# Kernel tuning notes

Hardware: AMD Instinct MI355X
Metric: run time of the kernel (lower is better)

## Reference

```python
import jax, jax.numpy as jnp
import numpy as np

N_NODES = 10000
N_EDGES = 160000
MUL = 16            # multiplicity: emb_dim=64, max_l=1 -> irreps 16x0e + 16x1o
EMB = 64
NUM_BASIS = 10
MAX_RADIUS = 4.5
HIDDEN = 64
N_PATHS = 4         # (0e,0e->0e), (0e,1o->1o), (1o,0e->1o), (1o,1o->0e)
W_NUMEL = N_PATHS * MUL * MUL  # 1024


def setup_inputs() -> dict:
    key = jax.random.key(0)
    ks = jax.random.split(key, 6)
    x = jax.random.normal(ks[0], (N_NODES, EMB), jnp.float32)
    src = jax.random.randint(ks[1], (N_EDGES,), 0, N_NODES)
    dst = jax.random.randint(ks[2], (N_EDGES,), 0, N_NODES)
    edge_vec = jax.random.normal(ks[3], (N_EDGES, 3), jnp.float32)
    mlp_w1 = jax.random.normal(ks[4], (NUM_BASIS, HIDDEN), jnp.float32)
    mlp_w2 = jax.random.normal(ks[5], (HIDDEN, W_NUMEL), jnp.float32)
    return {"x": x, "edge_vec": edge_vec, "mlp_w1": mlp_w1,
            "mlp_w2": mlp_w2, "src": src, "dst": dst}


def _sus(t):
    # e3nn smooth bump helper: exp(-1/t) for t>0 else 0
    return jnp.where(t > 0, jnp.exp(-1.0 / jnp.where(t > 0, t, 1.0)), 0.0)


def _radial_embedding(r):
    # soft_one_hot_linspace(basis='smooth_finite', cutoff=True), then *sqrt(num_basis)
    values = jnp.linspace(0.0, MAX_RADIUS, NUM_BASIS + 2)[1:-1]
    step = MAX_RADIUS / (NUM_BASIS + 1)
    diff = (r[:, None] - values) / step                     # [E, NUM_BASIS]
    basis = 1.14136 * jnp.exp(2.0) * _sus(diff + 1.0) * _sus(1.0 - diff)
    return basis * (NUM_BASIS ** 0.5)


def _forward(x, edge_vec, mlp_w1, mlp_w2, src, dst):
    E = edge_vec.shape[0]
    N = x.shape[0]
    r = jnp.linalg.norm(edge_vec, axis=1)                   # [E]
    # spherical harmonics, lmax=1, normalize=True, 'component' norm: Y0=1, Y1=sqrt(3)*n
    y1 = jnp.sqrt(3.0) * edge_vec / r[:, None]              # [E, 3]

    # radial MLP (e3nn FullyConnectedNet: W~N(0,1), x@W/sqrt(fan_in), relu scaled by sqrt(2))
    emb = _radial_embedding(r)                              # [E, 10]
    h = jnp.sqrt(2.0) * jax.nn.relu(emb @ (mlp_w1 / NUM_BASIS ** 0.5))
    w = h @ (mlp_w2 / HIDDEN ** 0.5)                        # [E, 1024]
    w = w.reshape(E, N_PATHS, MUL, MUL)                     # paths in e3nn order A,B,C,D

    xs = x[src]                                             # gather [E, 64]
    x0 = xs[:, :MUL]                                        # [E, 16] 0e scalars
    x1 = xs[:, MUL:].reshape(E, MUL, 3)                     # [E, 16, 3] 1o vectors

    # Fully connected TP normalization ('component', path_norm 'element'):
    # out0 fan = 2*MUL -> alpha 1/(2*MUL); out1 alpha 3/(2*MUL) with w3j 1/sqrt(3)
    c = 1.0 / jnp.sqrt(2.0 * MUL)
    inv_sqrt3 = 1.0 / jnp.sqrt(3.0)
    wA, wB, wC, wD = w[:, 0], w[:, 1], w[:, 2], w[:, 3]
    # 0e outputs: 0e*0e->0e and 1o*1o->0e (dot product, w3j = I/sqrt(3))
    out0 = c * (jnp.einsum('euw,eu->ew', wA, x0)
                + inv_sqrt3 * jnp.einsum('euw,eum,em->ew', wD, x1, y1))
    # 1o outputs: 0e*1o->1o and 1o*0e->1o (w3j = I/sqrt(3), Y0 = 1)
    out1 = c * (jnp.einsum('euw,eu,em->ewm', wB, x0, y1)
                + jnp.einsum('euw,eum->ewm', wC, x1))
    summand = jnp.concatenate([out0, out1.reshape(E, MUL * 3)], axis=1)  # [E, 64]

    out = jax.ops.segment_sum(summand, dst, num_segments=N)             # [N, 64]
    return out * (N / E)


def reference(x, edge_vec, mlp_w1, mlp_w2, src, dst):
    return _forward(x, edge_vec, mlp_w1, mlp_w2, src, dst)
```

## Files before the change

### kernel.cpp

```cpp
#include <hip/hip_runtime.h>
#include <hip/hip_bf16.h>


typedef __attribute__((ext_vector_type(8))) short bf16x8;
typedef __attribute__((ext_vector_type(8))) unsigned short u16x8;
typedef __attribute__((ext_vector_type(4))) float f32x4;

#define NN 10000
#define NE 160000

__device__ __forceinline__ float sus_f(float t) { return t > 0.0f ? __expf(-1.0f / t) : 0.0f; }
__device__ __forceinline__ unsigned int f2bf(float f) {
    unsigned int u = __float_as_uint(f);
    u += 0x7FFFu + ((u >> 16) & 1u);
    return u >> 16;
}
__device__ __forceinline__ float bf2f(unsigned short v) { return __uint_as_float(((unsigned int)v) << 16); }
__device__ __forceinline__ float bflo(unsigned int v) { return __uint_as_float(v << 16); }
__device__ __forceinline__ float bfhi(unsigned int v) { return __uint_as_float(v & 0xFFFF0000u); }
__device__ __forceinline__ float bfe(u16x8 v, int i) { return __uint_as_float(((unsigned int)v[i]) << 16); }

#define GL16(g, l) __builtin_amdgcn_global_load_lds( \
    (const __attribute__((address_space(1))) void*)(g), \
    (__attribute__((address_space(3))) void*)(l), 16, 0, 0)

__device__ __forceinline__ void stageN(const void* g, void* l, int bytes, int tid, int nthr) {
    const char* gc = (const char*)g;
    char* lc = (char*)l;
    const int units = bytes >> 4;
    for (int u = tid; u < units; u += nthr) GL16(gc + ((long)u << 4), lc + (u << 4));
}

__global__ void hist_k(const int* __restrict__ dst, int* __restrict__ hist,
                       const float* __restrict__ w2, char* __restrict__ w2bf) {
    if (blockIdx.x < 625) {
        const int e = blockIdx.x * 256 + threadIdx.x;
        if (e < NE) atomicAdd(&hist[dst[e]], 1);
    } else {
        const int idx = (blockIdx.x - 625) * 256 + threadIdx.x;
        const int j = idx >> 10, R = idx & 1023;
        unsigned int pk[4];
        #pragma unroll
        for (int p = 0; p < 4; ++p) {
            const unsigned int lo = f2bf(w2[(size_t)(8 * j + 2 * p) * 1024 + R]);
            const unsigned int hi = f2bf(w2[(size_t)(8 * j + 2 * p + 1) * 1024 + R]);
            pk[p] = lo | (hi << 16);
        }
        uint4 v; v.x = pk[0]; v.y = pk[1]; v.z = pk[2]; v.w = pk[3];
        *(uint4*)(w2bf + R * 128 + ((j ^ (R & 7)) << 4)) = v;
    }
}

__global__ __launch_bounds__(1024) void scan_k(const int* __restrict__ hist,
                                               int* __restrict__ offsets) {
    __shared__ int hl[NN];
    __shared__ int wsum[16];
    const int tid = threadIdx.x;
    for (int i = tid; i < NN; i += 1024) hl[i] = hist[i];
    __syncthreads();
    const int base = tid * 10;
    int loc[10]; int s = 0;
    #pragma unroll
    for (int i = 0; i < 10; ++i) { loc[i] = s; const int b = base + i; s += (b < NN) ? hl[b] : 0; }
    int v = s;
    const int lane = tid & 63, wv = tid >> 6;
    #pragma unroll
    for (int d = 1; d < 64; d <<= 1) { int t2 = __shfl_up(v, d); if (lane >= d) v += t2; }
    if (lane == 63) wsum[wv] = v;
    __syncthreads();
    if (tid < 64) {
        int w = (tid < 16) ? wsum[tid] : 0;
        #pragma unroll
        for (int d = 1; d < 16; d <<= 1) { int t2 = __shfl_up(w, d); if (tid >= d) w += t2; }
        if (tid < 16) wsum[tid] = w;
    }
    __syncthreads();
    const int wexc = (wv == 0) ? 0 : wsum[wv - 1];
    const int texc = wexc + v - s;
    #pragma unroll
    for (int i = 0; i < 10; ++i) { const int b = base + i; if (b < NN) offsets[b] = texc + loc[i]; }
    if (tid == 1023) offsets[NN] = texc + s;
}

__global__ void scatter_k(const int* __restrict__ dst, const int* __restrict__ src,
                          const int* __restrict__ offsets,
                          int* __restrict__ cursor, int* __restrict__ perm,
                          int* __restrict__ dsts, int* __restrict__ srcg) {
    const int e = blockIdx.x * 256 + threadIdx.x;
    if (e < NE) {
        const int d = dst[e];
        const int pos = offsets[d] + atomicAdd(&cursor[d], 1);
        perm[pos] = e;
        dsts[pos] = d;
        if (srcg) srcg[pos] = src[e];
    }
}

__global__ __launch_bounds__(512, 2) void se3_edge(
    const char* __restrict__ w2bf, const float* __restrict__ x,
    const float* __restrict__ edge_vec, const float* __restrict__ w1,
    const int* __restrict__ perm, const int* __restrict__ srcg,
    const int* __restrict__ dsts, float* __restrict__ out)
{
    __shared__ __align__(16) char w2lds[65536];
    __shared__ __align__(16) char x0l[4096];
    __shared__ __align__(16) char x1Tl[16384];
    __shared__ float y1l[128][4];
    __shared__ float embl[128][10];
    __shared__ __align__(16) float w1l[640];
    __shared__ __align__(16) int meta[1920];
    __shared__ __align__(16) char summb[12672];
    __shared__ int segst[2][66];
    __shared__ int nseg[2];

    const int tid = threadIdx.x, lane = tid & 63, wv = tid >> 6;
    const int lm = lane & 15, q = lane >> 4, erow = wv << 4;
    const int tb = blockIdx.x;
    const int pair = blockIdx.y;
    const int s0 = (q ^ (lm & 7)) << 4, s1 = s0 ^ 64;
    const int sel = tid >> 2, sa = tid & 3;
    const float S = 0.17677669529663687f * 0.125f * 0.0625f;
    const float C0 = 1.14136f * __expf(2.0f) * 3.1622776601683795f;
    const long e00 = (long)tb * 640;

    {
        const int pa = pair ? 1 : 0, pb = pair ? 2 : 3;
        stageN(w2bf + pa * 32768, w2lds, 32768, tid, 512);
        stageN(w2bf + pb * 32768, w2lds + 32768, 32768, tid, 512);
        stageN((const char*)(perm + e00), meta,        2560, tid, 512);
        stageN((const char*)(srcg + e00), meta + 640,  2560, tid, 512);
        stageN((const char*)(dsts + e00), meta + 1280, 2560, tid, 512);
        stageN((const char*)w1, w1l, 2560, tid, 512);
    }
    __syncthreads();

    const char* w2p0 = w2lds;
    const char* w2p1 = w2lds + 32768;
    const int arow = erow + lm;

    for (int tt = 0; tt < 5; ++tt) {
        const int eb = tt << 7;
        {
            const int eid = meta[eb + sel];
            const int s   = meta[640 + eb + sel];
            const float vx = edge_vec[eid * 3 + 0];
            const float vy = edge_vec[eid * 3 + 1];
            const float vz = edge_vec[eid * 3 + 2];
            const float r = sqrtf(vx * vx + vy * vy + vz * vz);
            if (sa == 0) {
                const float sc = 1.7320508075688772f / r;
                *(float4*)&y1l[sel][0] = make_float4(vx * sc, vy * sc, vz * sc, 0.f);
            }
            #pragma unroll
            for (int i = sa; i < 10; i += 4) {
                const float diff = r * (11.0f / 4.5f) - (float)(i + 1);
                embl[sel][i] = C0 * sus_f(diff + 1.0f) * sus_f(1.0f - diff);
            }
            const float4 v0 = *(const float4*)&x[(size_t)s * 64 + 4 * sa];
            uint2 p0;
            p0.x = f2bf(v0.x) | (f2bf(v0.y) << 16);
            p0.y = f2bf(v0.z) | (f2bf(v0.w) << 16);
            *(uint2*)(x0l + sel * 32 + sa * 8) = p0;
            const float* xp = &x[(size_t)s * 64 + 16 + 12 * sa];
            const float4 q0 = *(const float4*)xp;
            const float4 q1 = *(const float4*)(xp + 4);
            const float4 q2 = *(const float4*)(xp + 8);
            const float f[12] = { q0.x, q0.y, q0.z, q0.w, q1.x, q1.y,
                                  q1.z, q1.w, q2.x, q2.y, q2.z, q2.w };
            #pragma unroll
            for (int k = 0; k < 4; ++k) {
                uint2 v;
                v.x = f2bf(f[3 * k]) | (f2bf(f[3 * k + 1]) << 16);
                v.y = f2bf(f[3 * k + 2]);
                *(uint2*)(x1Tl + (((4 * sa + k) << 7) + sel) * 8) = v;
            }
        }
        __syncthreads();

        float ha[8], hb[8];
        #pragma unroll
        for (int jj = 0; jj < 8; ++jj) { ha[jj] = 0.f; hb[jj] = 0.f; }
        #pragma unroll
        for (int i = 0; i < 10; ++i) {
            const float ei = embl[arow][i];
            const float4 wa0 = *(const float4*)&w1l[i * 64 + 8 * q];
            const float4 wa1 = *(const float4*)&w1l[i * 64 + 8 * q + 4];
            const float4 wb0 = *(const float4*)&w1l[i * 64 + 32 + 8 * q];
            const float4 wb1 = *(const float4*)&w1l[i * 64 + 36 + 8 * q];
            ha[0] += ei * wa0.x; ha[1] += ei * wa0.y; ha[2] += ei * wa0.z; ha[3] += ei * wa0.w;
            ha[4] += ei * wa1.x; ha[5] += ei * wa1.y; ha[6] += ei * wa1.z; ha[7] += ei * wa1.w;
            hb[0] += ei * wb0.x; hb[1] += ei * wb0.y; hb[2] += ei * wb0.z; hb[3] += ei * wb0.w;
            hb[4] += ei * wb1.x; hb[5] += ei * wb1.y; hb[6] += ei * wb1.z; hb[7] += ei * wb1.w;
        }
        bf16x8 a0, a1;
        #pragma unroll
        for (int jj = 0; jj < 8; ++jj) {
            a0[jj] = (short)f2bf(fmaxf(ha[jj], 0.0f) * 0.4472135954999579f);
            a1[jj] = (short)f2bf(fmaxf(hb[jj], 0.0f) * 0.4472135954999579f);
        }

        u16x8 flo[4], fhi[4];
        float4 ye[4];
        #pragma unroll
        for (int r = 0; r < 4; ++r) {
            const int el = erow + 4 * q + r;
            flo[r] = *(const u16x8*)(x0l + el * 32);
            fhi[r] = *(const u16x8*)(x0l + el * 32 + 16);
            ye[r]  = *(const float4*)&y1l[el][0];
        }

        float ac0[4] = {0,0,0,0}, ac1[4] = {0,0,0,0}, ac2[4] = {0,0,0,0}, ac3[4] = {0,0,0,0};
        #pragma unroll
        for (int t = 0; t < 16; ++t) {
            const int rowb = (t * 16 + lm) << 7;
            const bf16x8 b00 = *(const bf16x8*)(w2p0 + rowb + s0);
            const bf16x8 b01 = *(const bf16x8*)(w2p0 + rowb + s1);
            const bf16x8 b10 = *(const bf16x8*)(w2p1 + rowb + s0);
            const bf16x8 b11 = *(const bf16x8*)(w2p1 + rowb + s1);
            f32x4 wP = {0.f,0.f,0.f,0.f}, wQ = {0.f,0.f,0.f,0.f};
            wP = __builtin_amdgcn_mfma_f32_16x16x32_bf16(a0, b00, wP, 0,0,0);
            wP = __builtin_amdgcn_mfma_f32_16x16x32_bf16(a1, b01, wP, 0,0,0);
            wQ = __builtin_amdgcn_mfma_f32_16x16x32_bf16(a0, b10, wQ, 0,0,0);
            wQ = __builtin_amdgcn_mfma_f32_16x16x32_bf16(a1, b11, wQ, 0,0,0);
            #pragma unroll
            for (int r = 0; r < 4; ++r) {
                const int el = erow + 4 * q + r;
                const uint2 xv = *(const uint2*)(x1Tl + (((t << 7) + el)) * 8);
                const float x0v = (t < 8) ? bfe(flo[r], t) : bfe(fhi[r], t - 8);
                ac0[r] += wP[r] * x0v;
                if (pair == 0) {
                    const float zv = bflo(xv.x) * ye[r].x + bfhi(xv.x) * ye[r].y
                                   + bflo(xv.y) * ye[r].z;
                    ac1[r] += wQ[r] * zv;
                } else {
                    ac1[r] += wQ[r] * bflo(xv.x);
                    ac2[r] += wQ[r] * bfhi(xv.x);
                    ac3[r] += wQ[r] * bflo(xv.y);
                }
            }
        }

        if (pair == 0) {
            float* summ32 = (float*)summb;
            #pragma unroll
            for (int r = 0; r < 4; ++r) {
                const int el = erow + 4 * q + r;
                summ32[lm * 132 + el] = S * (ac0[r] + 0.5773502691896258f * ac1[r]);
            }
        } else {
            unsigned short* summ16 = (unsigned short*)summb;
            #pragma unroll
            for (int r = 0; r < 4; ++r) {
                const int el = erow + 4 * q + r;
                const float b = S * ac0[r];
                summ16[(3 * lm + 0) * 132 + el] = (unsigned short)f2bf(b * ye[r].x + S * ac1[r]);
                summ16[(3 * lm + 1) * 132 + el] = (unsigned short)f2bf(b * ye[r].y + S * ac2[r]);
                summ16[(3 * lm + 2) * 132 + el] = (unsigned short)f2bf(b * ye[r].z + S * ac3[r]);
            }
        }
        const int* dstl = meta + 1280 + eb;
        if (wv < 2) {
            const int base = wv << 6;
            const int d = dstl[base + lane];
            const bool flag = (lane == 0) || (d != dstl[base + lane - 1]);
            const unsigned long long m = __ballot(flag);
            const int sid = (lane == 0) ? 0 : __popcll(m & ((1ull << lane) - 1ull));
            if (flag) segst[wv][sid] = base + lane;
            if (lane == 63) { const int ns = __popcll(m); nseg[wv] = ns; segst[wv][ns] = base + 64; }
        }
        __syncthreads();

        const int nsa = nseg[0], nsb = nseg[1];
        if (pair == 0) {
            const float* sm = (const float*)summb;
            const int total = (nsa + nsb) << 4;
            for (int i = tid; i < total; i += 512) {
                const int sg = i >> 4, c = i & 15;
                const int hh = (sg >= nsa) ? 1 : 0;
                const int sl = hh ? sg - nsa : sg;
                const int ebg = segst[hh][sl], ee = segst[hh][sl + 1];
                float s = 0.f;
                for (int e = ebg; e < ee; ++e) s += sm[c * 132 + e];
                atomicAdd(&out[(size_t)dstl[ebg] * 64 + c], s);
            }
        } else {
            const unsigned short* sm = (const unsigned short*)summb;
            const int total = (nsa + nsb) * 48;
            for (int i = tid; i < total; i += 512) {
                const int sg = i / 48, c = i - sg * 48;
                const int hh = (sg >= nsa) ? 1 : 0;
                const int sl = hh ? sg - nsa : sg;
                const int ebg = segst[hh][sl], ee = segst[hh][sl + 1];
                float s = 0.f;
                for (int e = ebg; e < ee; ++e) s += bf2f(sm[c * 132 + e]);
                atomicAdd(&out[(size_t)dstl[ebg] * 64 + 16 + c], s);
            }
        }
    }
}

#define FBT 64
template<int PATH>
__device__ __forceinline__ void fb_body(
    const float* __restrict__ x, const float* __restrict__ edge_vec,
    const float* __restrict__ w1, const float* __restrict__ w2,
    const int* __restrict__ src, const int* __restrict__ perm,
    const int* __restrict__ dsts, float* __restrict__ out,
    unsigned short (*w2t)[72], float* arena, float (*y1l)[4],
    int* dstl, int* srcl, int* segstart, int* nseg_s)
{
    constexpr int NC    = (PATH == 0 || PATH == 3) ? 16 : 48;
    constexpr int CBASE = (PATH == 0 || PATH == 3) ? 0 : 16;
    const int tid = threadIdx.x;
    float* embl = arena;
    unsigned short* hl = (unsigned short*)(arena + 640);
    float* feats = arena + 2944;
    float* summ  = arena;
    {
        const float* col = w2 + PATH * 256 + tid;
        #pragma unroll
        for (int k = 0; k < 64; k += 2) {
            const unsigned int lo = f2bf(col[(size_t)k * 1024]);
            const unsigned int hi = f2bf(col[(size_t)(k + 1) * 1024]);
            *(unsigned int*)&w2t[tid][k] = lo | (hi << 16);
        }
    }
    const int lane = tid & 63, wv = tid >> 6, lm = lane & 15, q = lane >> 4;
    const int erow = wv * 16;
    const float C0 = 1.14136f * __expf(2.0f) * 3.1622776601683795f;
    const float S  = 0.17677669529663687f * 0.125f * 0.0625f;
    for (int it = 0; it < 2; ++it) {
        const int e0 = (blockIdx.x * 2 + it) * FBT;
        __syncthreads();
        for (int idx = tid; idx < FBT * 10; idx += 256) {
            const int e = idx / 10, i = idx - e * 10;
            const int eid = perm[e0 + e];
            const float vx = edge_vec[eid * 3 + 0], vy = edge_vec[eid * 3 + 1], vz = edge_vec[eid * 3 + 2];
            const float r = sqrtf(vx * vx + vy * vy + vz * vz);
            const float diff = r * (11.0f / 4.5f) - (float)(i + 1);
            embl[e * 10 + i] = C0 * sus_f(diff + 1.0f) * sus_f(1.0f - diff);
            if (i == 0) {
                const float sc = 1.7320508075688772f / r;
                y1l[e][0] = vx * sc; y1l[e][1] = vy * sc; y1l[e][2] = vz * sc;
                dstl[e] = dsts[e0 + e];
                srcl[e] = src[eid];
            }
        }
        __syncthreads();
        for (int idx = tid; idx < FBT * 8; idx += 256) {
            const int e = idx >> 3, j0 = (idx & 7) * 8;
            float acc[8];
            #pragma unroll
            for (int j = 0; j < 8; ++j) acc[j] = 0.0f;
            #pragma unroll
            for (int i = 0; i < 10; ++i) {
                const float ei = embl[e * 10 + i];
                #pragma unroll
                for (int j = 0; j < 8; ++j) acc[j] += ei * w1[i * 64 + j0 + j];
            }
            unsigned int pk[4];
            #pragma unroll
            for (int p = 0; p < 4; ++p) {
                const unsigned int lo = f2bf(fmaxf(acc[2 * p],     0.0f) * 0.4472135954999579f);
                const unsigned int hi = f2bf(fmaxf(acc[2 * p + 1], 0.0f) * 0.4472135954999579f);
                pk[p] = lo | (hi << 16);
            }
            uint4 v; v.x = pk[0]; v.y = pk[1]; v.z = pk[2]; v.w = pk[3];
            *(uint4*)&hl[e * 72 + j0] = v;
        }
        if (PATH == 2) {
            for (int idx = tid; idx < FBT * 48; idx += 256) {
                const int e = idx / 48, c = idx - e * 48;
                feats[e * 48 + c] = x[(size_t)srcl[e] * 64 + 16 + c];
            }
        } else if (PATH == 3) {
            for (int idx = tid; idx < FBT * 16; idx += 256) {
                const int e = idx >> 4, u = idx & 15;
                const float* xs = x + (size_t)srcl[e] * 64 + 16 + u * 3;
                feats[e * 16 + u] = xs[0] * y1l[e][0] + xs[1] * y1l[e][1] + xs[2] * y1l[e][2];
            }
        } else {
            for (int idx = tid; idx < FBT * 16; idx += 256) {
                const int e = idx >> 4, u = idx & 15;
                feats[e * 16 + u] = x[(size_t)srcl[e] * 64 + u];
            }
        }
        __syncthreads();
        const bf16x8 a0 = *(const bf16x8*)&hl[(erow + lm) * 72 + 8 * q];
        const bf16x8 a1 = *(const bf16x8*)&hl[(erow + lm) * 72 + 32 + 8 * q];
        float accO[4] = {0.f,0.f,0.f,0.f}, accC0[4] = {0.f,0.f,0.f,0.f};
        float accC1[4] = {0.f,0.f,0.f,0.f}, accC2[4] = {0.f,0.f,0.f,0.f};
        #pragma unroll 4
        for (int t = 0; t < 16; ++t) {
            const bf16x8 b0 = *(const bf16x8*)&w2t[t * 16 + lm][8 * q];
            const bf16x8 b1 = *(const bf16x8*)&w2t[t * 16 + lm][32 + 8 * q];
            f32x4 wa = {0.f,0.f,0.f,0.f};
            wa = __builtin_amdgcn_mfma_f32_16x16x32_bf16(a0, b0, wa, 0, 0, 0);
            wa = __builtin_amdgcn_mfma_f32_16x16x32_bf16(a1, b1, wa, 0, 0, 0);
            #pragma unroll
            for (int r = 0; r < 4; ++r) {
                const int el = erow + 4 * q + r;
                if (PATH == 2) {
                    accC0[r] += wa[r] * feats[el * 48 + t * 3 + 0];
                    accC1[r] += wa[r] * feats[el * 48 + t * 3 + 1];
                    accC2[r] += wa[r] * feats[el * 48 + t * 3 + 2];
                } else {
                    accO[r] += wa[r] * feats[el * 16 + t];
                }
            }
        }
        __syncthreads();
        #pragma unroll
        for (int r = 0; r < 4; ++r) {
            const int el = erow + 4 * q + r;
            if (PATH == 0) summ[el * 16 + lm] = S * accO[r];
            else if (PATH == 3) summ[el * 16 + lm] = S * 0.5773502691896258f * accO[r];
            else if (PATH == 1) {
                const float tv = S * accO[r];
                summ[el * 48 + lm * 3 + 0] = tv * y1l[el][0];
                summ[el * 48 + lm * 3 + 1] = tv * y1l[el][1];
                summ[el * 48 + lm * 3 + 2] = tv * y1l[el][2];
            } else {
                summ[el * 48 + lm * 3 + 0] = S * accC0[r];
                summ[el * 48 + lm * 3 + 1] = S * accC1[r];
                summ[el * 48 + lm * 3 + 2] = S * accC2[r];
            }
        }
        if (tid < 64) {
            const int d = dstl[tid];
            const bool flag = (tid == 0) || (d != dstl[tid - 1]);
            const unsigned long long m = __ballot(flag);
            const int sid = (tid == 0) ? 0 : __popcll(m & ((1ull << tid) - 1ull));
            if (flag) segstart[sid] = tid;
            if (tid == 63) { const int ns = __popcll(m); *nseg_s = ns; segstart[ns] = 64; }
        }
        __syncthreads();
        const int ns = *nseg_s;
        for (int i = tid; i < ns * NC; i += 256) {
            const int s = i / NC, c = i - s * NC;
            const int eb = segstart[s], ee = segstart[s + 1];
            float sum = 0.0f;
            for (int e = eb; e < ee; ++e) sum += summ[e * NC + c];
            atomicAdd(&out[(size_t)dstl[eb] * 64 + CBASE + c], sum);
        }
    }
}

__global__ __launch_bounds__(256, 2) void fb_edge(
    const float* __restrict__ x, const float* __restrict__ edge_vec,
    const float* __restrict__ w1, const float* __restrict__ w2,
    const int* __restrict__ src, const int* __restrict__ perm,
    const int* __restrict__ dsts, float* __restrict__ out)
{
    __shared__ unsigned short w2t[256][72];
    __shared__ float arena[6016];
    __shared__ float y1l[FBT][4];
    __shared__ int dstl[FBT];
    __shared__ int srcl[FBT];
    __shared__ int segstart[FBT + 1];
    __shared__ int nseg_s;
    switch (blockIdx.y) {
        case 0:  fb_body<0>(x, edge_vec, w1, w2, src, perm, dsts, out, w2t, arena, y1l, dstl, srcl, segstart, &nseg_s); break;
        case 1:  fb_body<1>(x, edge_vec, w1, w2, src, perm, dsts, out, w2t, arena, y1l, dstl, srcl, segstart, &nseg_s); break;
        case 2:  fb_body<2>(x, edge_vec, w1, w2, src, perm, dsts, out, w2t, arena, y1l, dstl, srcl, segstart, &nseg_s); break;
        default: fb_body<3>(x, edge_vec, w1, w2, src, perm, dsts, out, w2t, arena, y1l, dstl, srcl, segstart, &nseg_s); break;
    }
}

extern "C" void kernel_launch(void* const* d_in, const int* in_sizes, int n_in,
                              void* d_out, int out_size, void* d_ws, size_t ws_size,
                              hipStream_t stream) {
    const float* x        = (const float*)d_in[0];
    const float* edge_vec = (const float*)d_in[1];
    const float* w1       = (const float*)d_in[2];
    const float* w2       = (const float*)d_in[3];
    const int*   src      = (const int*)d_in[4];
    const int*   dst      = (const int*)d_in[5];
    float* out = (float*)d_out;

    char* ws = (char*)d_ws;
    size_t off = 0;
    auto alloc = [&](size_t n) -> char* {
        off = (off + 255) & ~(size_t)255;
        char* p = ws + off; off += n; return p;
    };
    int* hist    = (int*)alloc(40000);
    int* cursor  = (int*)alloc(40000);
    int* offsets = (int*)alloc(40004);
    int* perm    = (int*)alloc(640000);
    int* dsts    = (int*)alloc(640000);
    int* srcg    = (int*)alloc(640000);
    char* w2bf   = alloc(131072);
    const bool big = (off <= ws_size);

    hipMemsetAsync(d_out, 0, (size_t)out_size * sizeof(float), stream);
    hipMemsetAsync(d_ws, 0, 81408, stream);

    if (big) {
        hipLaunchKernelGGL(hist_k, dim3(657), dim3(256), 0, stream, dst, hist, w2, w2bf);
        hipLaunchKernelGGL(scan_k, dim3(1), dim3(1024), 0, stream, hist, offsets);
        hipLaunchKernelGGL(scatter_k, dim3(625), dim3(256), 0, stream,
                           dst, src, offsets, cursor, perm, dsts, srcg);
        hipLaunchKernelGGL(se3_edge, dim3(250, 2), dim3(512), 0, stream,
                           w2bf, x, edge_vec, w1, perm, srcg, dsts, out);
    } else {
        hipLaunchKernelGGL(hist_k, dim3(625), dim3(256), 0, stream, dst, hist, w2, w2bf);
        hipLaunchKernelGGL(scan_k, dim3(1), dim3(1024), 0, stream, hist, offsets);
        hipLaunchKernelGGL(scatter_k, dim3(625), dim3(256), 0, stream,
                           dst, src, offsets, cursor, perm, dsts, (int*)nullptr);
        hipLaunchKernelGGL(fb_edge, dim3(1250, 4), dim3(256), 0, stream,
                           x, edge_vec, w1, w2, src, perm, dsts, out);
    }
}
```

Measured before the change: 153.5 us.

## Split the two weight paths across wave slices in 1024-thread edge blocks

Doubles the block size to 1024 threads and assigns each of the two paths handled per block to a separate group of eight waves, each with its own LDS partial-sum buffer. The two buffers are summed during the segmented scatter. For pair 0 the 1o·y dot product is now computed once during staging rather than inside the MFMA loop, which shortens the per-edge inner loops. In exchange it uses more LDS and registers per block, and half the threads sit idle during the staging phase. The launch bounds hint 4 blocks per CU, which LDS use may not permit.

```diff
diff --git a/kernel.cpp b/kernel.cpp
--- a/kernel.cpp
+++ b/kernel.cpp
@@ -96,7 +96,7 @@
     }
 }
 
-__global__ __launch_bounds__(512, 2) void se3_edge(
+__global__ __launch_bounds__(1024, 4) void se3_edge(
     const char* __restrict__ w2bf, const float* __restrict__ x,
     const float* __restrict__ edge_vec, const float* __restrict__ w1,
     const int* __restrict__ perm, const int* __restrict__ srcg,
@@ -104,17 +104,19 @@
 {
     __shared__ __align__(16) char w2lds[65536];
     __shared__ __align__(16) char x0l[4096];
-    __shared__ __align__(16) char x1Tl[16384];
+    __shared__ __align__(16) char fb[16640];
     __shared__ float y1l[128][4];
     __shared__ float embl[128][10];
     __shared__ __align__(16) float w1l[640];
     __shared__ __align__(16) int meta[1920];
-    __shared__ __align__(16) char summb[12672];
+    __shared__ __align__(16) char summb[2][12672];
     __shared__ int segst[2][66];
     __shared__ int nseg[2];
 
     const int tid = threadIdx.x, lane = tid & 63, wv = tid >> 6;
-    const int lm = lane & 15, q = lane >> 4, erow = wv << 4;
+    const int lm = lane & 15, q = lane >> 4;
+    const int mt = wv & 7, slice = wv >> 3;
+    const int erow = mt << 4;
     const int tb = blockIdx.x;
     const int pair = blockIdx.y;
     const int s0 = (q ^ (lm & 7)) << 4, s1 = s0 ^ 64;
@@ -125,33 +127,30 @@
 
     {
         const int pa = pair ? 1 : 0, pb = pair ? 2 : 3;
-        stageN(w2bf + pa * 32768, w2lds, 32768, tid, 512);
-        stageN(w2bf + pb * 32768, w2lds + 32768, 32768, tid, 512);
-        stageN((const char*)(perm + e00), meta,        2560, tid, 512);
-        stageN((const char*)(srcg + e00), meta + 640,  2560, tid, 512);
-        stageN((const char*)(dsts + e00), meta + 1280, 2560, tid, 512);
-        stageN((const char*)w1, w1l, 2560, tid, 512);
+        stageN(w2bf + pa * 32768, w2lds, 32768, tid, 1024);
+        stageN(w2bf + pb * 32768, w2lds + 32768, 32768, tid, 1024);
+        stageN((const char*)(perm + e00), meta,        2560, tid, 1024);
+        stageN((const char*)(srcg + e00), meta + 640,  2560, tid, 1024);
+        stageN((const char*)(dsts + e00), meta + 1280, 2560, tid, 1024);
+        stageN((const char*)w1, w1l, 2560, tid, 1024);
     }
     __syncthreads();
 
-    const char* w2p0 = w2lds;
-    const char* w2p1 = w2lds + 32768;
+    const char* w2p = w2lds + slice * 32768;
     const int arow = erow + lm;
 
     for (int tt = 0; tt < 5; ++tt) {
         const int eb = tt << 7;
-        {
+        if (tid < 512) {
             const int eid = meta[eb + sel];
             const int s   = meta[640 + eb + sel];
             const float vx = edge_vec[eid * 3 + 0];
             const float vy = edge_vec[eid * 3 + 1];
             const float vz = edge_vec[eid * 3 + 2];
             const float r = sqrtf(vx * vx + vy * vy + vz * vz);
-            if (sa == 0) {
-                const float sc = 1.7320508075688772f / r;
+            const float sc = 1.7320508075688772f / r;
+            if (sa == 0)
                 *(float4*)&y1l[sel][0] = make_float4(vx * sc, vy * sc, vz * sc, 0.f);
-            }
-            #pragma unroll
             for (int i = sa; i < 10; i += 4) {
                 const float diff = r * (11.0f / 4.5f) - (float)(i + 1);
                 embl[sel][i] = C0 * sus_f(diff + 1.0f) * sus_f(1.0f - diff);
@@ -167,12 +166,23 @@
             const float4 q2 = *(const float4*)(xp + 8);
             const float f[12] = { q0.x, q0.y, q0.z, q0.w, q1.x, q1.y,
                                   q1.z, q1.w, q2.x, q2.y, q2.z, q2.w };
-            #pragma unroll
-            for (int k = 0; k < 4; ++k) {
-                uint2 v;
-                v.x = f2bf(f[3 * k]) | (f2bf(f[3 * k + 1]) << 16);
-                v.y = f2bf(f[3 * k + 2]);
-                *(uint2*)(x1Tl + (((4 * sa + k) << 7) + sel) * 8) = v;
+            if (pair == 0) {
+                unsigned int zp[2];
+                #pragma unroll
+                for (int h = 0; h < 2; ++h) {
+                    const float za = (f[6*h+0] * vx + f[6*h+1] * vy + f[6*h+2] * vz) * sc;
+                    const float zb = (f[6*h+3] * vx + f[6*h+4] * vy + f[6*h+5] * vz) * sc;
+                    zp[h] = f2bf(za) | (f2bf(zb) << 16);
+                }
+                *(uint2*)(fb + sel * 32 + sa * 8) = make_uint2(zp[0], zp[1]);
+            } else {
+                #pragma unroll
+                for (int k = 0; k < 4; ++k) {
+                    uint2 v;
+                    v.x = f2bf(f[3 * k]) | (f2bf(f[3 * k + 1]) << 16);
+                    v.y = f2bf(f[3 * k + 2]);
+                    *(uint2*)(fb + (4 * sa + k) * 1040 + sel * 8) = v;
+                }
             }
         }
         __syncthreads();
@@ -199,65 +209,78 @@
             a1[jj] = (short)f2bf(fmaxf(hb[jj], 0.0f) * 0.4472135954999579f);
         }
 
-        u16x8 flo[4], fhi[4];
-        float4 ye[4];
-        #pragma unroll
-        for (int r = 0; r < 4; ++r) {
-            const int el = erow + 4 * q + r;
-            flo[r] = *(const u16x8*)(x0l + el * 32);
-            fhi[r] = *(const u16x8*)(x0l + el * 32 + 16);
-            ye[r]  = *(const float4*)&y1l[el][0];
-        }
-
-        float ac0[4] = {0,0,0,0}, ac1[4] = {0,0,0,0}, ac2[4] = {0,0,0,0}, ac3[4] = {0,0,0,0};
-        #pragma unroll
-        for (int t = 0; t < 16; ++t) {
-            const int rowb = (t * 16 + lm) << 7;
-            const bf16x8 b00 = *(const bf16x8*)(w2p0 + rowb + s0);
-            const bf16x8 b01 = *(const bf16x8*)(w2p0 + rowb + s1);
-            const bf16x8 b10 = *(const bf16x8*)(w2p1 + rowb + s0);
-            const bf16x8 b11 = *(const bf16x8*)(w2p1 + rowb + s1);
-            f32x4 wP = {0.f,0.f,0.f,0.f}, wQ = {0.f,0.f,0.f,0.f};
-            wP = __builtin_amdgcn_mfma_f32_16x16x32_bf16(a0, b00, wP, 0,0,0);
-            wP = __builtin_amdgcn_mfma_f32_16x16x32_bf16(a1, b01, wP, 0,0,0);
-            wQ = __builtin_amdgcn_mfma_f32_16x16x32_bf16(a0, b10, wQ, 0,0,0);
-            wQ = __builtin_amdgcn_mfma_f32_16x16x32_bf16(a1, b11, wQ, 0,0,0);
+        if (pair == 0 || slice == 0) {
+            const char* f16b = (slice == 0) ? x0l : fb;
+            u16x8 flo[4], fhi[4];
+            float4 ye[4];
             #pragma unroll
             for (int r = 0; r < 4; ++r) {
                 const int el = erow + 4 * q + r;
-                const uint2 xv = *(const uint2*)(x1Tl + (((t << 7) + el)) * 8);
-                const float x0v = (t < 8) ? bfe(flo[r], t) : bfe(fhi[r], t - 8);
-                ac0[r] += wP[r] * x0v;
-                if (pair == 0) {
-                    const float zv = bflo(xv.x) * ye[r].x + bfhi(xv.x) * ye[r].y
-                                   + bflo(xv.y) * ye[r].z;
-                    ac1[r] += wQ[r] * zv;
-                } else {
-                    ac1[r] += wQ[r] * bflo(xv.x);
-                    ac2[r] += wQ[r] * bfhi(xv.x);
-                    ac3[r] += wQ[r] * bflo(xv.y);
+                flo[r] = *(const u16x8*)(f16b + el * 32);
+                fhi[r] = *(const u16x8*)(f16b + el * 32 + 16);
+                if (pair == 1) ye[r] = *(const float4*)&y1l[el][0];
+            }
+            float ac[4] = {0.f, 0.f, 0.f, 0.f};
+            #pragma unroll
+            for (int t = 0; t < 16; ++t) {
+                const int rowb = (t * 16 + lm) << 7;
+                const bf16x8 b0 = *(const bf16x8*)(w2p + rowb + s0);
+                const bf16x8 b1 = *(const bf16x8*)(w2p + rowb + s1);
+                f32x4 w = {0.f, 0.f, 0.f, 0.f};
+                w = __builtin_amdgcn_mfma_f32_16x16x32_bf16(a0, b0, w, 0, 0, 0);
+                w = __builtin_amdgcn_mfma_f32_16x16x32_bf16(a1, b1, w, 0, 0, 0);
+                #pragma unroll
+                for (int r = 0; r < 4; ++r)
+                    ac[r] += w[r] * (t < 8 ? bfe(flo[r], t) : bfe(fhi[r], t - 8));
+            }
+            if (pair == 0) {
+                const float scl = (slice == 0) ? S : S * 0.5773502691896258f;
+                float* pl = (float*)summb[slice];
+                #pragma unroll
+                for (int r = 0; r < 4; ++r) {
+                    const int el = erow + 4 * q + r;
+                    pl[lm * 132 + el] = scl * ac[r];
                 }
-            }
-        }
-
-        if (pair == 0) {
-            float* summ32 = (float*)summb;
+            } else {
+                unsigned short* pl = (unsigned short*)summb[0];
+                #pragma unroll
+                for (int r = 0; r < 4; ++r) {
+                    const int el = erow + 4 * q + r;
+                    const float b = S * ac[r];
+                    pl[(3 * lm + 0) * 132 + el] = (unsigned short)f2bf(b * ye[r].x);
+                    pl[(3 * lm + 1) * 132 + el] = (unsigned short)f2bf(b * ye[r].y);
+                    pl[(3 * lm + 2) * 132 + el] = (unsigned short)f2bf(b * ye[r].z);
+                }
+            }
+        } else {
+            float ac1[4] = {0,0,0,0}, ac2[4] = {0,0,0,0}, ac3[4] = {0,0,0,0};
+            #pragma unroll
+            for (int t = 0; t < 16; ++t) {
+                const int rowb = (t * 16 + lm) << 7;
+                const bf16x8 b0 = *(const bf16x8*)(w2p + rowb + s0);
+                const bf16x8 b1 = *(const bf16x8*)(w2p + rowb + s1);
+                f32x4 w = {0.f, 0.f, 0.f, 0.f};
+                w = __builtin_amdgcn_mfma_f32_16x16x32_bf16(a0, b0, w, 0, 0, 0);
+                w = __builtin_amdgcn_mfma_f32_16x16x32_bf16(a1, b1, w, 0, 0, 0);
+                #pragma unroll
+                for (int r = 0; r < 4; ++r) {
+                    const int el = erow + 4 * q + r;
+                    const uint2 xv = *(const uint2*)(fb + t * 1040 + el * 8);
+                    ac1[r] += w[r] * bflo(xv.x);
+                    ac2[r] += w[r] * bfhi(xv.x);
+                    ac3[r] += w[r] * bflo(xv.y);
+                }
+            }
+            unsigned short* pl = (unsigned short*)summb[1];
             #pragma unroll
             for (int r = 0; r < 4; ++r) {
                 const int el = erow + 4 * q + r;
-                summ32[lm * 132 + el] = S * (ac0[r] + 0.5773502691896258f * ac1[r]);
-            }
-        } else {
-            unsigned short* summ16 = (unsigned short*)summb;
-            #pragma unroll
-            for (int r = 0; r < 4; ++r) {
-                const int el = erow + 4 * q + r;
-                const float b = S * ac0[r];
-                summ16[(3 * lm + 0) * 132 + el] = (unsigned short)f2bf(b * ye[r].x + S * ac1[r]);
-                summ16[(3 * lm + 1) * 132 + el] = (unsigned short)f2bf(b * ye[r].y + S * ac2[r]);
-                summ16[(3 * lm + 2) * 132 + el] = (unsigned short)f2bf(b * ye[r].z + S * ac3[r]);
-            }
-        }
+                pl[(3 * lm + 0) * 132 + el] = (unsigned short)f2bf(S * ac1[r]);
+                pl[(3 * lm + 1) * 132 + el] = (unsigned short)f2bf(S * ac2[r]);
+                pl[(3 * lm + 2) * 132 + el] = (unsigned short)f2bf(S * ac3[r]);
+            }
+        }
+
         const int* dstl = meta + 1280 + eb;
         if (wv < 2) {
             const int base = wv << 6;
@@ -272,27 +295,30 @@
 
         const int nsa = nseg[0], nsb = nseg[1];
         if (pair == 0) {
-            const float* sm = (const float*)summb;
+            const float* p0 = (const float*)summb[0];
+            const float* p1 = (const float*)summb[1];
             const int total = (nsa + nsb) << 4;
-            for (int i = tid; i < total; i += 512) {
+            for (int i = tid; i < total; i += 1024) {
                 const int sg = i >> 4, c = i & 15;
                 const int hh = (sg >= nsa) ? 1 : 0;
                 const int sl = hh ? sg - nsa : sg;
                 const int ebg = segst[hh][sl], ee = segst[hh][sl + 1];
                 float s = 0.f;
-                for (int e = ebg; e < ee; ++e) s += sm[c * 132 + e];
+                for (int e = ebg; e < ee; ++e) s += p0[c * 132 + e] + p1[c * 132 + e];
                 atomicAdd(&out[(size_t)dstl[ebg] * 64 + c], s);
             }
         } else {
-            const unsigned short* sm = (const unsigned short*)summb;
+            const unsigned short* p0 = (const unsigned short*)summb[0];
+            const unsigned short* p1 = (const unsigned short*)summb[1];
             const int total = (nsa + nsb) * 48;
-            for (int i = tid; i < total; i += 512) {
+            for (int i = tid; i < total; i += 1024) {
                 const int sg = i / 48, c = i - sg * 48;
                 const int hh = (sg >= nsa) ? 1 : 0;
                 const int sl = hh ? sg - nsa : sg;
                 const int ebg = segst[hh][sl], ee = segst[hh][sl + 1];
                 float s = 0.f;
-                for (int e = ebg; e < ee; ++e) s += bf2f(sm[c * 132 + e]);
+                for (int e = ebg; e < ee; ++e)
+                    s += bf2f(p0[c * 132 + e]) + bf2f(p1[c * 132 + e]);
                 atomicAdd(&out[(size_t)dstl[ebg] * 64 + 16 + c], s);
             }
         }
@@ -501,7 +527,7 @@
         hipLaunchKernelGGL(scan_k, dim3(1), dim3(1024), 0, stream, hist, offsets);
         hipLaunchKernelGGL(scatter_k, dim3(625), dim3(256), 0, stream,
                            dst, src, offsets, cursor, perm, dsts, srcg);
-        hipLaunchKernelGGL(se3_edge, dim3(250, 2), dim3(512), 0, stream,
+        hipLaunchKernelGGL(se3_edge, dim3(250, 2), dim3(1024), 0, stream,
                            w2bf, x, edge_vec, w1, perm, srcg, dsts, out);
     } else {
         hipLaunchKernelGGL(hist_k, dim3(625), dim3(256), 0, stream, dst, hist, w2, w2bf);
```

Measured after the change: 158.6 us. 3.3% more time.
